# Kernel optimization log

Hardware: AMD Instinct MI355X
Metric: run time of the kernel (lower is better)

## Reference

```python
import jax, jax.numpy as jnp
import numpy as np

N = 100000        # nodes
E = 1600000       # edges (avg degree 16)
D = 128           # feature dim (in_dim == out_dim)
L = 3             # num_layers
P = 8             # num_parts


def setup_inputs() -> dict:
    key = jax.random.key(0)
    k1, k2, k3, k4, k5, k6 = jax.random.split(key, 6)
    edge_row = jnp.sort(jax.random.randint(k1, (E,), 0, N))
    edge_col = jax.random.randint(k2, (E,), 0, N)
    edge_vals = jax.random.uniform(k3, (E,), dtype=jnp.float32)
    x = jax.random.normal(k4, (N, D), dtype=jnp.float32)
    stacked_params = jax.random.normal(k5, (L, D, D, P), dtype=jnp.float32)
    layer_weights = jax.random.normal(k6, (L, P), dtype=jnp.float32)
    return {"edge_row": edge_row, "edge_col": edge_col, "edge_vals": edge_vals,
            "x": x, "stacked_params": stacked_params, "layer_weights": layer_weights}


def reference(edge_row, edge_col, edge_vals, x, stacked_params, layer_weights):
    n = x.shape[0]
    num_layers = stacked_params.shape[0]
    h = x
    for i in range(num_layers):
        # sparse adj.spmm(h): gather source features, scale by edge value, sum per row
        msg = h[edge_col] * edge_vals[:, None]                       # [E, D]
        ax = jax.ops.segment_sum(msg, edge_row, num_segments=n)      # [N, D]
        # MyLinear: softmax over the num_parts weight, contract parts dim
        w = jax.nn.softmax(layer_weights[i])                         # [P]
        ww = jnp.einsum('oip,p->oi', stacked_params[i], w)           # [D_out, D_in]
        h = ax @ ww.T                                                # [N, D_out]
        if i < num_layers - 1:
            h = jax.nn.relu(h)
    return h
```

## Files before the change

kernel.cpp:

```cpp
#include <hip/hip_runtime.h>
#include <cstdint>

#define D 128
#define P 8
#define L 3

typedef __attribute__((ext_vector_type(8))) _Float16 f16x8;
typedef __attribute__((ext_vector_type(4))) float    f32x4;

__global__ void build_row_ptr(const int* __restrict__ er, int* __restrict__ rp, int n, int e) {
    int r = blockIdx.x * blockDim.x + threadIdx.x;
    if (r > n) return;
    int lo = 0, hi = e;
    while (lo < hi) {
        int mid = (lo + hi) >> 1;
        if (er[mid] < r) lo = mid + 1; else hi = mid;
    }
    rp[r] = lo;
}

__global__ void build_ww(const float* __restrict__ sp, const float* __restrict__ lw,
                         _Float16* __restrict__ wwB) {
    int idx = blockIdx.x * blockDim.x + threadIdx.x;
    if (idx >= L * D * D) return;
    int l = idx / (D * D);
    int rem = idx - l * D * D;
    int o = rem / D;
    int i = rem - o * D;
    float wv[P];
    float m = -1e30f;
#pragma unroll
    for (int p = 0; p < P; p++) { wv[p] = lw[l * P + p]; m = fmaxf(m, wv[p]); }
    float s = 0.f;
#pragma unroll
    for (int p = 0; p < P; p++) { wv[p] = __expf(wv[p] - m); s += wv[p]; }
    float inv = 1.0f / s;
    const float* spp = sp + ((size_t)(l * D + o) * D + i) * P;
    float acc = 0.f;
#pragma unroll
    for (int p = 0; p < P; p++) acc += spp[p] * wv[p];
    int kt = i >> 5, kp = i & 31;
    wwB[(((l * 4 + kt) * D + o) << 5) + kp] = (_Float16)(acc * inv);
}

static __device__ __forceinline__ void mfma_store16(const _Float16 (*s_h)[136],
                                                    const _Float16* __restrict__ wwB_l,
                                                    _Float16* __restrict__ y,
                                                    int row0, int n, int tid) {
    const int w = tid >> 6, lane = tid & 63;
    const int quad = lane >> 4, l16 = lane & 15;
    f32x4 acc[2] = {};
#pragma unroll
    for (int kt = 0; kt < 4; kt++) {
        f16x8 af = *(const f16x8*)&s_h[l16][kt * 32 + quad * 8];
#pragma unroll
        for (int c = 0; c < 2; c++) {
            const int ct = w * 2 + c;
            f16x8 bf = *(const f16x8*)&wwB_l[((kt * D + ct * 16 + l16) << 5) + quad * 8];
            acc[c] = __builtin_amdgcn_mfma_f32_16x16x32_f16(af, bf, acc[c], 0, 0, 0);
        }
    }
#pragma unroll
    for (int c = 0; c < 2; c++) {
        const int ct = w * 2 + c;
#pragma unroll
        for (int rg = 0; rg < 4; rg++) {
            int row = row0 + quad * 4 + rg;
            if (row < n) y[row * D + ct * 16 + l16] = (_Float16)acc[c][rg];
        }
    }
}

__global__ __launch_bounds__(256, 8)
void gemm_x32(const float* __restrict__ x, const _Float16* __restrict__ wwB_l,
              _Float16* __restrict__ y, int n) {
    __shared__ _Float16 s_h[16][136];
    const int tid = threadIdx.x;
    const int row0 = blockIdx.x * 16;
    const int c8 = (tid & 15) * 8;
    {
        int r = tid >> 4;
        int row = row0 + r;
        float4 v0 = {}, v1 = {};
        if (row < n) {
            v0 = *(const float4*)&x[row * D + c8];
            v1 = *(const float4*)&x[row * D + c8 + 4];
        }
        f16x8 h;
        h[0] = (_Float16)v0.x; h[1] = (_Float16)v0.y;
        h[2] = (_Float16)v0.z; h[3] = (_Float16)v0.w;
        h[4] = (_Float16)v1.x; h[5] = (_Float16)v1.y;
        h[6] = (_Float16)v1.z; h[7] = (_Float16)v1.w;
        *(f16x8*)&s_h[r][c8] = h;
    }
    __syncthreads();
    mfma_store16(s_h, wwB_l, y, row0, n, tid);
}

static __device__ __forceinline__ void gather_row(float (&a)[8],
                                                  const _Float16* __restrict__ y,
                                                  const int* __restrict__ col,
                                                  const float* __restrict__ vals,
                                                  int e, int e1, int c8) {
    union U8 { uint4 u; _Float16 h[8]; };
    for (; e + 8 <= e1; e += 8) {
        int c[8]; float v[8]; U8 g[8];
#pragma unroll
        for (int j = 0; j < 8; j++) { c[j] = col[e + j]; v[j] = vals[e + j]; }
#pragma unroll
        for (int j = 0; j < 8; j++) g[j].u = *(const uint4*)&y[c[j] * D + c8];
#pragma unroll
        for (int j = 0; j < 8; j++)
#pragma unroll
            for (int k = 0; k < 8; k++) a[k] += v[j] * (float)g[j].h[k];
    }
    for (; e + 4 <= e1; e += 4) {
        int c[4]; float v[4]; U8 g[4];
#pragma unroll
        for (int j = 0; j < 4; j++) { c[j] = col[e + j]; v[j] = vals[e + j]; }
#pragma unroll
        for (int j = 0; j < 4; j++) g[j].u = *(const uint4*)&y[c[j] * D + c8];
#pragma unroll
        for (int j = 0; j < 4; j++)
#pragma unroll
            for (int k = 0; k < 8; k++) a[k] += v[j] * (float)g[j].h[k];
    }
    for (; e < e1; e++) {
        U8 g; g.u = *(const uint4*)&y[col[e] * D + c8];
        float v = vals[e];
#pragma unroll
        for (int k = 0; k < 8; k++) a[k] += v * (float)g.h[k];
    }
}

__global__ __launch_bounds__(256, 8)
void fused_layer(const _Float16* __restrict__ yprev, const int* __restrict__ rp,
                 const int* __restrict__ col, const float* __restrict__ vals,
                 const _Float16* __restrict__ wwB_l, _Float16* __restrict__ ynext, int n) {
    __shared__ _Float16 s_h[16][136];
    const int tid = threadIdx.x;
    const int row0 = blockIdx.x * 16;
    const int sg = tid >> 4;
    const int c8 = (tid & 15) * 8;
    {
        int r = row0 + sg;
        float a[8] = {0.f, 0.f, 0.f, 0.f, 0.f, 0.f, 0.f, 0.f};
        if (r < n) gather_row(a, yprev, col, vals, rp[r], rp[r + 1], c8);
        f16x8 o;
#pragma unroll
        for (int k = 0; k < 8; k++) o[k] = (_Float16)fmaxf(a[k], 0.f);
        *(f16x8*)&s_h[sg][c8] = o;
    }
    __syncthreads();
    mfma_store16(s_h, wwB_l, ynext, row0, n, tid);
}

__global__ __launch_bounds__(256, 8)
void spmm_f32(const _Float16* __restrict__ y, const int* __restrict__ rp,
              const int* __restrict__ col, const float* __restrict__ vals,
              float* __restrict__ out, int n) {
    const int tid = threadIdx.x;
    const int r = blockIdx.x * 16 + (tid >> 4);
    const int c8 = (tid & 15) * 8;
    if (r >= n) return;
    float a[8] = {0.f, 0.f, 0.f, 0.f, 0.f, 0.f, 0.f, 0.f};
    gather_row(a, y, col, vals, rp[r], rp[r + 1], c8);
    *(float4*)&out[r * D + c8]     = make_float4(a[0], a[1], a[2], a[3]);
    *(float4*)&out[r * D + c8 + 4] = make_float4(a[4], a[5], a[6], a[7]);
}

extern "C" void kernel_launch(void* const* d_in, const int* in_sizes, int n_in,
                              void* d_out, int out_size, void* d_ws, size_t ws_size,
                              hipStream_t stream) {
    const int*   edge_row  = (const int*)d_in[0];
    const int*   edge_col  = (const int*)d_in[1];
    const float* edge_vals = (const float*)d_in[2];
    const float* x         = (const float*)d_in[3];
    const float* sp        = (const float*)d_in[4];
    const float* lw        = (const float*)d_in[5];
    float* out = (float*)d_out;

    const int E_ = in_sizes[0];
    const int N_ = in_sizes[3] / D;

    char* ws = (char*)d_ws;
    int* row_ptr = (int*)ws;
    size_t off = (((size_t)(N_ + 1) * sizeof(int)) + 255) & ~(size_t)255;
    _Float16* wwB = (_Float16*)(ws + off);
    off += (size_t)L * 4 * D * 32 * sizeof(_Float16);
    off = (off + 255) & ~(size_t)255;
    _Float16* bufA = (_Float16*)(ws + off);
    off += (size_t)N_ * D * sizeof(_Float16);
    _Float16* bufB = (_Float16*)(ws + off);

    build_row_ptr<<<(N_ + 1 + 255) / 256, 256, 0, stream>>>(edge_row, row_ptr, N_, E_);
    build_ww<<<(L * D * D + 255) / 256, 256, 0, stream>>>(sp, lw, wwB);

    const int sblk = (N_ + 15) / 16;
    const int WWL = 4 * D * 32;

    gemm_x32<<<sblk, 256, 0, stream>>>(x, wwB, bufA, N_);
    fused_layer<<<sblk, 256, 0, stream>>>(bufA, row_ptr, edge_col, edge_vals,
                                          wwB + WWL,     bufB, N_);
    fused_layer<<<sblk, 256, 0, stream>>>(bufB, row_ptr, edge_col, edge_vals,
                                          wwB + 2 * WWL, bufA, N_);
    spmm_f32<<<sblk, 256, 0, stream>>>(bufA, row_ptr, edge_col, edge_vals, out, N_);
}
```

Baseline: 316.8 us.

## Balance edge work across thread groups in fused layer with shared-memory atomics

The fused gather+GEMM layer kernel now splits the block's edge range evenly across its 16 thread groups instead of giving each group one row. Partial row sums are flushed into an fp32 shared accumulator with atomic adds whenever a row boundary is crossed. ReLU and the fp16 conversion are applied when the MFMA operands are loaded. This targets load imbalance from variable row degrees, at the cost of shared-memory atomics, a zero-init pass and a larger fp32 shared buffer that may lower occupancy.

```diff
diff --git a/kernel.cpp b/kernel.cpp
--- a/kernel.cpp
+++ b/kernel.cpp
@@ -97,6 +97,98 @@
     mfma_store16(s_h, wwB_l, y, row0, n, tid);
 }
 
+__global__ __launch_bounds__(256, 8)
+void fused_layer(const _Float16* __restrict__ yprev, const int* __restrict__ rp,
+                 const int* __restrict__ col, const float* __restrict__ vals,
+                 const _Float16* __restrict__ wwB_l, _Float16* __restrict__ ynext, int n) {
+    __shared__ float s_acc[16][132];
+    __shared__ int   s_rp[17];
+    const int tid = threadIdx.x;
+    const int row0 = blockIdx.x * 16;
+    if (tid < 17) {
+        int r = row0 + tid;
+        s_rp[tid] = rp[r < n ? r : n];
+    }
+    for (int i = tid; i < 16 * 132; i += 256) (&s_acc[0][0])[i] = 0.f;
+    __syncthreads();
+
+    const int sg = tid >> 4;
+    const int c8 = (tid & 15) * 8;
+    const int te0 = s_rp[0], te1 = s_rp[16];
+    const int chunk = (te1 - te0 + 15) >> 4;
+    int e = te0 + sg * chunk;
+    const int e1 = min(e + chunk, te1);
+
+    union U8 { uint4 u; _Float16 h[8]; };
+    if (e < e1) {
+        int cur = 0;
+        while (s_rp[cur + 1] <= e) cur++;
+        int rp_next = s_rp[cur + 1];
+        float a[8] = {0.f, 0.f, 0.f, 0.f, 0.f, 0.f, 0.f, 0.f};
+        for (; e + 8 <= e1; e += 8) {
+            int c[8]; float v[8]; U8 g[8];
+#pragma unroll
+            for (int j = 0; j < 8; j++) { c[j] = col[e + j]; v[j] = vals[e + j]; }
+#pragma unroll
+            for (int j = 0; j < 8; j++) g[j].u = *(const uint4*)&yprev[c[j] * D + c8];
+#pragma unroll
+            for (int j = 0; j < 8; j++) {
+                while (e + j >= rp_next) {
+#pragma unroll
+                    for (int k = 0; k < 8; k++) {
+                        atomicAdd(&s_acc[cur][c8 + k], a[k]); a[k] = 0.f;
+                    }
+                    cur++; rp_next = s_rp[cur + 1];
+                }
+#pragma unroll
+                for (int k = 0; k < 8; k++) a[k] += v[j] * (float)g[j].h[k];
+            }
+        }
+        for (; e < e1; e++) {
+            U8 g; g.u = *(const uint4*)&yprev[col[e] * D + c8];
+            float v = vals[e];
+            while (e >= rp_next) {
+#pragma unroll
+                for (int k = 0; k < 8; k++) {
+                    atomicAdd(&s_acc[cur][c8 + k], a[k]); a[k] = 0.f;
+                }
+                cur++; rp_next = s_rp[cur + 1];
+            }
+#pragma unroll
+            for (int k = 0; k < 8; k++) a[k] += v * (float)g.h[k];
+        }
+#pragma unroll
+        for (int k = 0; k < 8; k++) atomicAdd(&s_acc[cur][c8 + k], a[k]);
+    }
+    __syncthreads();
+
+    const int w = tid >> 6, lane = tid & 63;
+    const int quad = lane >> 4, l16 = lane & 15;
+    f32x4 acc[2] = {};
+#pragma unroll
+    for (int kt = 0; kt < 4; kt++) {
+        const float* src = &s_acc[l16][kt * 32 + quad * 8];
+        f16x8 af;
+#pragma unroll
+        for (int k = 0; k < 8; k++) af[k] = (_Float16)fmaxf(src[k], 0.f);
+#pragma unroll
+        for (int c = 0; c < 2; c++) {
+            const int ct = w * 2 + c;
+            f16x8 bf = *(const f16x8*)&wwB_l[((kt * D + ct * 16 + l16) << 5) + quad * 8];
+            acc[c] = __builtin_amdgcn_mfma_f32_16x16x32_f16(af, bf, acc[c], 0, 0, 0);
+        }
+    }
+#pragma unroll
+    for (int c = 0; c < 2; c++) {
+        const int ct = w * 2 + c;
+#pragma unroll
+        for (int rg = 0; rg < 4; rg++) {
+            int row = row0 + quad * 4 + rg;
+            if (row < n) ynext[row * D + ct * 16 + l16] = (_Float16)acc[c][rg];
+        }
+    }
+}
+
 static __device__ __forceinline__ void gather_row(float (&a)[8],
                                                   const _Float16* __restrict__ y,
                                                   const int* __restrict__ col,
@@ -131,28 +223,6 @@
 #pragma unroll
         for (int k = 0; k < 8; k++) a[k] += v * (float)g.h[k];
     }
-}
-
-__global__ __launch_bounds__(256, 8)
-void fused_layer(const _Float16* __restrict__ yprev, const int* __restrict__ rp,
-                 const int* __restrict__ col, const float* __restrict__ vals,
-                 const _Float16* __restrict__ wwB_l, _Float16* __restrict__ ynext, int n) {
-    __shared__ _Float16 s_h[16][136];
-    const int tid = threadIdx.x;
-    const int row0 = blockIdx.x * 16;
-    const int sg = tid >> 4;
-    const int c8 = (tid & 15) * 8;
-    {
-        int r = row0 + sg;
-        float a[8] = {0.f, 0.f, 0.f, 0.f, 0.f, 0.f, 0.f, 0.f};
-        if (r < n) gather_row(a, yprev, col, vals, rp[r], rp[r + 1], c8);
-        f16x8 o;
-#pragma unroll
-        for (int k = 0; k < 8; k++) o[k] = (_Float16)fmaxf(a[k], 0.f);
-        *(f16x8*)&s_h[sg][c8] = o;
-    }
-    __syncthreads();
-    mfma_store16(s_h, wwB_l, ynext, row0, n, tid);
 }
 
 __global__ __launch_bounds__(256, 8)
```

Result: slower. 478.6 us (+51.0%).

## Sort rows by degree into a permutation for balanced SpMM blocks

Applied to the files above, without the earlier changes.

Adds a degree histogram, scan and counting-sort pass that builds a permutation of rows ordered by descending degree. The SpMM and fused layer kernels then process permuted rows, so each 16-row block groups rows of similar degree and per-block load imbalance shrinks. In exchange it adds four small kernels with atomics per call, an extra indirection on every row read and write, and scattered output stores. With random degrees around 16 the imbalance to recover may be small.

```diff
diff --git a/kernel.cpp b/kernel.cpp
--- a/kernel.cpp
+++ b/kernel.cpp
@@ -4,6 +4,7 @@
 #define D 128
 #define P 8
 #define L 3
+#define BINS 256
 
 typedef __attribute__((ext_vector_type(8))) _Float16 f16x8;
 typedef __attribute__((ext_vector_type(4))) float    f32x4;
@@ -17,6 +18,38 @@
         if (er[mid] < r) lo = mid + 1; else hi = mid;
     }
     rp[r] = lo;
+}
+
+__global__ void zero_hist(int* __restrict__ hist) {
+    hist[threadIdx.x] = 0;
+}
+__global__ void hist_deg(const int* __restrict__ rp, int* __restrict__ hist, int n) {
+    int r = blockIdx.x * blockDim.x + threadIdx.x;
+    if (r >= n) return;
+    int d = min(rp[r + 1] - rp[r], BINS - 1);
+    atomicAdd(&hist[(BINS - 1) - d], 1);
+}
+__global__ void scan_hist(int* __restrict__ hist) {
+    __shared__ int a[BINS], b[BINS];
+    int t = threadIdx.x;
+    int orig = hist[t];
+    a[t] = orig;
+    __syncthreads();
+    int* src = a; int* dst = b;
+    for (int off = 1; off < BINS; off <<= 1) {
+        dst[t] = src[t] + ((t >= off) ? src[t - off] : 0);
+        __syncthreads();
+        int* tmp = src; src = dst; dst = tmp;
+    }
+    hist[t] = src[t] - orig;
+}
+__global__ void build_perm(const int* __restrict__ rp, int* __restrict__ hist,
+                           int* __restrict__ perm, int n) {
+    int r = blockIdx.x * blockDim.x + threadIdx.x;
+    if (r >= n) return;
+    int d = min(rp[r + 1] - rp[r], BINS - 1);
+    int pos = atomicAdd(&hist[(BINS - 1) - d], 1);
+    perm[pos] = r;
 }
 
 __global__ void build_ww(const float* __restrict__ sp, const float* __restrict__ lw,
@@ -43,10 +76,11 @@
     wwB[(((l * 4 + kt) * D + o) << 5) + kp] = (_Float16)(acc * inv);
 }
 
-static __device__ __forceinline__ void mfma_store16(const _Float16 (*s_h)[136],
-                                                    const _Float16* __restrict__ wwB_l,
-                                                    _Float16* __restrict__ y,
-                                                    int row0, int n, int tid) {
+static __device__ __forceinline__ void mfma_store16p(const _Float16 (*s_h)[136],
+                                                     const _Float16* __restrict__ wwB_l,
+                                                     _Float16* __restrict__ y,
+                                                     const int* __restrict__ perm,
+                                                     int row0, int n, int tid) {
     const int w = tid >> 6, lane = tid & 63;
     const int quad = lane >> 4, l16 = lane & 15;
     f32x4 acc[2] = {};
@@ -65,8 +99,11 @@
         const int ct = w * 2 + c;
 #pragma unroll
         for (int rg = 0; rg < 4; rg++) {
-            int row = row0 + quad * 4 + rg;
-            if (row < n) y[row * D + ct * 16 + l16] = (_Float16)acc[c][rg];
+            int idx = row0 + quad * 4 + rg;
+            if (idx < n) {
+                int row = perm[idx];
+                y[row * D + ct * 16 + l16] = (_Float16)acc[c][rg];
+            }
         }
     }
 }
@@ -94,7 +131,29 @@
         *(f16x8*)&s_h[r][c8] = h;
     }
     __syncthreads();
-    mfma_store16(s_h, wwB_l, y, row0, n, tid);
+
+    const int w = tid >> 6, lane = tid & 63;
+    const int quad = lane >> 4, l16 = lane & 15;
+    f32x4 acc[2] = {};
+#pragma unroll
+    for (int kt = 0; kt < 4; kt++) {
+        f16x8 af = *(const f16x8*)&s_h[l16][kt * 32 + quad * 8];
+#pragma unroll
+        for (int c = 0; c < 2; c++) {
+            const int ct = w * 2 + c;
+            f16x8 bf = *(const f16x8*)&wwB_l[((kt * D + ct * 16 + l16) << 5) + quad * 8];
+            acc[c] = __builtin_amdgcn_mfma_f32_16x16x32_f16(af, bf, acc[c], 0, 0, 0);
+        }
+    }
+#pragma unroll
+    for (int c = 0; c < 2; c++) {
+        const int ct = w * 2 + c;
+#pragma unroll
+        for (int rg = 0; rg < 4; rg++) {
+            int row = row0 + quad * 4 + rg;
+            if (row < n) y[row * D + ct * 16 + l16] = (_Float16)acc[c][rg];
+        }
+    }
 }
 
 static __device__ __forceinline__ void gather_row(float (&a)[8],
@@ -136,6 +195,7 @@
 __global__ __launch_bounds__(256, 8)
 void fused_layer(const _Float16* __restrict__ yprev, const int* __restrict__ rp,
                  const int* __restrict__ col, const float* __restrict__ vals,
+                 const int* __restrict__ perm,
                  const _Float16* __restrict__ wwB_l, _Float16* __restrict__ ynext, int n) {
     __shared__ _Float16 s_h[16][136];
     const int tid = threadIdx.x;
@@ -143,26 +203,30 @@
     const int sg = tid >> 4;
     const int c8 = (tid & 15) * 8;
     {
-        int r = row0 + sg;
+        int idx = row0 + sg;
         float a[8] = {0.f, 0.f, 0.f, 0.f, 0.f, 0.f, 0.f, 0.f};
-        if (r < n) gather_row(a, yprev, col, vals, rp[r], rp[r + 1], c8);
+        if (idx < n) {
+            int r = perm[idx];
+            gather_row(a, yprev, col, vals, rp[r], rp[r + 1], c8);
+        }
         f16x8 o;
 #pragma unroll
         for (int k = 0; k < 8; k++) o[k] = (_Float16)fmaxf(a[k], 0.f);
         *(f16x8*)&s_h[sg][c8] = o;
     }
     __syncthreads();
-    mfma_store16(s_h, wwB_l, ynext, row0, n, tid);
+    mfma_store16p(s_h, wwB_l, ynext, perm, row0, n, tid);
 }
 
 __global__ __launch_bounds__(256, 8)
 void spmm_f32(const _Float16* __restrict__ y, const int* __restrict__ rp,
               const int* __restrict__ col, const float* __restrict__ vals,
-              float* __restrict__ out, int n) {
+              const int* __restrict__ perm, float* __restrict__ out, int n) {
     const int tid = threadIdx.x;
-    const int r = blockIdx.x * 16 + (tid >> 4);
+    const int idx = blockIdx.x * 16 + (tid >> 4);
     const int c8 = (tid & 15) * 8;
-    if (r >= n) return;
+    if (idx >= n) return;
+    const int r = perm[idx];
     float a[8] = {0.f, 0.f, 0.f, 0.f, 0.f, 0.f, 0.f, 0.f};
     gather_row(a, y, col, vals, rp[r], rp[r + 1], c8);
     *(float4*)&out[r * D + c8]     = make_float4(a[0], a[1], a[2], a[3]);
@@ -186,6 +250,10 @@
     char* ws = (char*)d_ws;
     int* row_ptr = (int*)ws;
     size_t off = (((size_t)(N_ + 1) * sizeof(int)) + 255) & ~(size_t)255;
+    int* hist = (int*)(ws + off);
+    off += (size_t)BINS * sizeof(int);
+    int* perm = (int*)(ws + off);
+    off = ((off + (size_t)N_ * sizeof(int)) + 255) & ~(size_t)255;
     _Float16* wwB = (_Float16*)(ws + off);
     off += (size_t)L * 4 * D * 32 * sizeof(_Float16);
     off = (off + 255) & ~(size_t)255;
@@ -193,16 +261,21 @@
     off += (size_t)N_ * D * sizeof(_Float16);
     _Float16* bufB = (_Float16*)(ws + off);
 
+    const int nb = (N_ + 255) / 256;
     build_row_ptr<<<(N_ + 1 + 255) / 256, 256, 0, stream>>>(edge_row, row_ptr, N_, E_);
+    zero_hist<<<1, BINS, 0, stream>>>(hist);
+    hist_deg<<<nb, 256, 0, stream>>>(row_ptr, hist, N_);
+    scan_hist<<<1, BINS, 0, stream>>>(hist);
+    build_perm<<<nb, 256, 0, stream>>>(row_ptr, hist, perm, N_);
     build_ww<<<(L * D * D + 255) / 256, 256, 0, stream>>>(sp, lw, wwB);
 
     const int sblk = (N_ + 15) / 16;
     const int WWL = 4 * D * 32;
 
     gemm_x32<<<sblk, 256, 0, stream>>>(x, wwB, bufA, N_);
-    fused_layer<<<sblk, 256, 0, stream>>>(bufA, row_ptr, edge_col, edge_vals,
+    fused_layer<<<sblk, 256, 0, stream>>>(bufA, row_ptr, edge_col, edge_vals, perm,
                                           wwB + WWL,     bufB, N_);
-    fused_layer<<<sblk, 256, 0, stream>>>(bufB, row_ptr, edge_col, edge_vals,
+    fused_layer<<<sblk, 256, 0, stream>>>(bufB, row_ptr, edge_col, edge_vals, perm,
                                           wwB + 2 * WWL, bufA, N_);
-    spmm_f32<<<sblk, 256, 0, stream>>>(bufA, row_ptr, edge_col, edge_vals, out, N_);
-}
+    spmm_f32<<<sblk, 256, 0, stream>>>(bufA, row_ptr, edge_col, edge_vals, perm, out, N_);
+}
```

Result: slower. 858.2 us (+170.9%).
